# Kernel optimization log

Measured on AMD Instinct MI355X. Metric: run time of the kernel, lower is better.

## Reference

```python
import jax, jax.numpy as jnp
import numpy as np

FULL_SCALE = 32.0
TOPK = 5
R = 0.5


def _match(ca, cb, fa, fb):
    # ca: [Na,3] int coords, cb: [Nb,3] int coords, fa: [Na,C], fb: [Nb,C]
    xa = ca.astype(jnp.float32)
    xb = cb.astype(jnp.float32)
    # pairwise L2 distance via the expanded form, clamped at 0 before sqrt
    d2 = ((xa * xa).sum(-1)[:, None]
          + (xb * xb).sum(-1)[None, :]
          - 2.0 * (xa @ xb.T))                     # [Na, Nb]
    dist = jnp.sqrt(jnp.maximum(d2, 0.0)) / FULL_SCALE
    # smallest-k distances == top-k of negated distances
    neg_top, idx = jax.lax.top_k(-dist, TOPK)      # idx: [Na, TOPK]
    dist_w = R - jnp.clip(-neg_top, 0.0, R)        # [Na, TOPK]
    gathered = fb[idx]                             # [Na, TOPK, C]
    matched = jnp.sum(gathered * dist_w[..., None], axis=1)  # [Na, C]
    return jnp.concatenate([fa, matched], axis=-1)  # [Na, 2C]


def setup_inputs() -> dict:
    key = jax.random.key(0)
    k1, k2, k3, k4 = jax.random.split(key, 4)
    B, Na, Nb, C = 4, 8192, 8192, 64
    coords_a = jax.random.randint(k1, (B, Na, 3), 0, 32, dtype=jnp.int32)
    coords_b = jax.random.randint(k2, (B, Nb, 3), 0, 32, dtype=jnp.int32)
    feat_a = jax.random.normal(k3, (B, Na, C), dtype=jnp.float32)
    feat_b = jax.random.normal(k4, (B, Nb, C), dtype=jnp.float32)
    return {"coords_a": coords_a, "coords_b": coords_b,
            "feat_a": feat_a, "feat_b": feat_b}


def reference(coords_a, coords_b, feat_a, feat_b):
    # vmap over independent point groups (the original's python loop over batch idx)
    return jax.vmap(_match)(coords_a, coords_b, feat_a, feat_b)  # [B, Na, 2C]
```

## Files before the change

### kernel.cpp

```cpp
#include <hip/hip_runtime.h>
#include <stdint.h>


namespace {
constexpr int kB = 4;
constexpr int kNa = 8192;
constexpr int kNb = 8192;
constexpr int kC = 64;

constexpr int kRad = 8;
constexpr int kDMax = 64;
constexpr int kGrid = 48;
constexpr int kGrid2 = kGrid * kGrid;
constexpr int kGrid3 = kGrid2 * kGrid;
constexpr int kOff = kRad * kGrid2 + kRad * kGrid + kRad;

constexpr int kChunkSz = 32;
constexpr int kMaxChunks = 128;
constexpr int kTabCap = kMaxChunks * kChunkSz;

constexpr int kOvfCap = 256;

constexpr size_t kCntOff    = 0;
constexpr size_t kOvfCntOff = 442368;
constexpr size_t kOvfIdxOff = 442372;
constexpr size_t kSlotLoOff = 443396;
constexpr size_t kSlotHiOff = kSlotLoOff + (size_t)kB * kGrid3 * 4;
constexpr size_t kWsWords   = kSlotHiOff + (size_t)kB * kGrid3 * 4;
constexpr size_t kWsBytes   = kWsWords * 4ull;

constexpr int kZeroVecEnd = (int)((kOvfCntOff + 4) / 4);
constexpr int kFFVecBeg   = (int)(kSlotLoOff / 4);
constexpr int kFFVecEnd   = (int)(kSlotHiOff / 4);
constexpr int kClrBlocks  = (kFFVecEnd + 255) / 256;

struct Tab {
    uint32_t e[kTabCap];
    unsigned long long canStop[2];
    int nChunks;
};
constexpr Tab buildTab() {
    Tab t{};
    for (int i = 0; i < kTabCap; ++i) t.e[i] = 0x7FFFFFFFu;
    t.canStop[0] = 0; t.canStop[1] = 0;
    int cnt[kDMax + 1] = {};
    for (int dx = -kRad; dx <= kRad; ++dx)
        for (int dy = -kRad; dy <= kRad; ++dy)
            for (int dz = -kRad; dz <= kRad; ++dz) {
                const int d2 = dx * dx + dy * dy + dz * dz;
                if (d2 <= kDMax) cnt[d2]++;
            }
    int pos[kDMax + 1] = {};
    int fill = 0;
    for (int d = 0; d <= kDMax; ++d) {
        if (cnt[d] == 0) { pos[d] = -1; continue; }
        const int room = kChunkSz - (fill % kChunkSz);
        if (room < cnt[d] && room != kChunkSz) fill += room;
        pos[d] = fill;
        fill += cnt[d];
    }
    t.nChunks = (fill + kChunkSz - 1) / kChunkSz;
    for (int dx = -kRad; dx <= kRad; ++dx)
        for (int dy = -kRad; dy <= kRad; ++dy)
            for (int dz = -kRad; dz <= kRad; ++dz) {
                const int d2 = dx * dx + dy * dy + dz * dz;
                if (d2 <= kDMax) {
                    const int sd = dx * kGrid2 + dy * kGrid + dz + kOff;
                    t.e[pos[d2]++] = ((uint32_t)d2 << 18) | (uint32_t)sd;
                }
            }
    for (int c = 0; c < t.nChunks; ++c) {
        int lastReal = -1;
        for (int i = (c + 1) * kChunkSz - 1; i >= 0; --i) {
            const unsigned d = t.e[i] >> 18;
            if (d <= (unsigned)kDMax) { lastReal = (int)d; break; }
        }
        int nextReal = kDMax + 1;
        for (int i = (c + 1) * kChunkSz; i < kTabCap; ++i) {
            const unsigned d = t.e[i] >> 18;
            if (d <= (unsigned)kDMax) { nextReal = (int)d; break; }
        }
        if (nextReal > lastReal) t.canStop[c >> 6] |= (1ull << (c & 63));
    }
    return t;
}
__device__ constexpr Tab kTab = buildTab();
constexpr int kNChunks = buildTab().nChunks;
constexpr unsigned long long kCS0 = buildTab().canStop[0];
constexpr unsigned long long kCS1 = buildTab().canStop[1];
static_assert(buildTab().nChunks <= kMaxChunks, "table overflow");
}

__device__ __forceinline__ uint32_t umin_(uint32_t a, uint32_t b) { return a < b ? a : b; }
__device__ __forceinline__ uint32_t umax_(uint32_t a, uint32_t b) { return a > b ? a : b; }

#define INSERT5(T0, T1, T2, T3, T4, KEY) do {                 \
    const uint32_t m0_ = umax_(T0, KEY); T0 = umin_(T0, KEY); \
    const uint32_t m1_ = umax_(T1, m0_); T1 = umin_(T1, m0_); \
    const uint32_t m2_ = umax_(T2, m1_); T2 = umin_(T2, m1_); \
    const uint32_t m3_ = umax_(T3, m2_); T3 = umin_(T3, m2_); \
    T4 = umin_(T4, m3_); } while (0)

__device__ __forceinline__ void merge5_(uint32_t& t0, uint32_t& t1, uint32_t& t2,
                                        uint32_t& t3, uint32_t& t4,
                                        uint32_t b0, uint32_t b1, uint32_t b2,
                                        uint32_t b3, uint32_t b4) {
    const uint32_t c0 = umin_(t0, b0);
    const uint32_t c1 = umin_(umin_(umax_(t0, b0), t1), b1);
    const uint32_t c2 = umin_(umin_(umax_(t0, b1), umax_(t1, b0)), umin_(t2, b2));
    const uint32_t c3 = umin_(umin_(umax_(t0, b2), umax_(t1, b1)),
                              umin_(umax_(t2, b0), umin_(t3, b3)));
    const uint32_t c4 = umin_(umin_(umax_(t0, b3), umax_(t1, b2)),
                              umin_(umin_(umax_(t2, b1), umax_(t3, b0)),
                                    umin_(t4, b4)));
    t0 = c0; t1 = c1; t2 = c2; t3 = c3; t4 = c4;
}

__device__ __forceinline__ void groupMerge5_(uint32_t& t0, uint32_t& t1, uint32_t& t2,
                                             uint32_t& t3, uint32_t& t4) {
    #pragma unroll
    for (int s = 1; s < 16; s <<= 1) {
        const uint32_t b0 = (uint32_t)__shfl_xor((int)t0, s);
        const uint32_t b1 = (uint32_t)__shfl_xor((int)t1, s);
        const uint32_t b2 = (uint32_t)__shfl_xor((int)t2, s);
        const uint32_t b3 = (uint32_t)__shfl_xor((int)t3, s);
        const uint32_t b4 = (uint32_t)__shfl_xor((int)t4, s);
        merge5_(t0, t1, t2, t3, t4, b0, b1, b2, b3, b4);
    }
}

__device__ __forceinline__ void waveMerge5_(uint32_t& t0, uint32_t& t1, uint32_t& t2,
                                            uint32_t& t3, uint32_t& t4) {
    #pragma unroll
    for (int s = 1; s < 64; s <<= 1) {
        const uint32_t b0 = (uint32_t)__shfl_xor((int)t0, s);
        const uint32_t b1 = (uint32_t)__shfl_xor((int)t1, s);
        const uint32_t b2 = (uint32_t)__shfl_xor((int)t2, s);
        const uint32_t b3 = (uint32_t)__shfl_xor((int)t3, s);
        const uint32_t b4 = (uint32_t)__shfl_xor((int)t4, s);
        merge5_(t0, t1, t2, t3, t4, b0, b1, b2, b3, b4);
    }
}


__global__ __launch_bounds__(256)
void k_clear(uint4* __restrict__ ws) {
    const int i = blockIdx.x * 256 + threadIdx.x;
    if (i < kZeroVecEnd) ws[i] = uint4{0u, 0u, 0u, 0u};
    else if (i >= kFFVecBeg && i < kFFVecEnd) ws[i] = uint4{~0u, ~0u, ~0u, ~0u};
}

__global__ void k_scatter(const int* __restrict__ coords_b,
                          uint32_t* __restrict__ cnt,
                          uint32_t* __restrict__ slotLo,
                          uint32_t* __restrict__ slotHi,
                          uint32_t* __restrict__ ovfCnt,
                          uint32_t* __restrict__ ovfIdx) {
    const int i = blockIdx.x * blockDim.x + threadIdx.x;
    if (i >= kB * kNb) return;
    const int b = i >> 13;
    const int j = i & (kNb - 1);
    const int* p = coords_b + (size_t)i * 3;
    const int cell = b * kGrid3
                   + (p[0] + kRad) * kGrid2 + (p[1] + kRad) * kGrid + (p[2] + kRad);
    const uint32_t pos = atomicAdd(&cnt[cell], 1u);
    if (pos < 4u) {
        slotLo[(size_t)cell * 4 + pos] = (uint32_t)j;
    } else if (pos < 8u) {
        slotHi[(size_t)cell * 4 + (pos - 4u)] = (uint32_t)j;
    } else {
        const uint32_t op = atomicAdd(&ovfCnt[b], 1u);
        if (op < (uint32_t)kOvfCap) ovfIdx[b * kOvfCap + op] = (uint32_t)j;
    }
}


__global__ __launch_bounds__(512, 8)
void dist_match_bucket(const int* __restrict__ coords_a,
                       const int* __restrict__ coords_b,
                       const float* __restrict__ feat_a,
                       const float* __restrict__ feat_b,
                       const uint32_t* __restrict__ cnt,
                       const uint32_t* __restrict__ slotLo,
                       const uint32_t* __restrict__ slotHi,
                       const uint32_t* __restrict__ ovfCnt,
                       const uint32_t* __restrict__ ovfIdx,
                       float* __restrict__ out)
{
    const int b = blockIdx.x >> 8;
    const int rowBase = (blockIdx.x & 255) * 32;
    const int lane = threadIdx.x & 63;
    const int wave = threadIdx.x >> 6;
    const int sub = lane & 15;
    const int grp = lane >> 4;
    const int row = rowBase + wave * 4 + grp;

    const int* ca = coords_a + ((size_t)b * kNa + row) * 3;
    const int ax = ca[0], ay = ca[1], az = ca[2];
    const int aCell = (ax + kRad) * kGrid2 + (ay + kRad) * kGrid + (az + kRad);
    const int base = b * kGrid3 + aCell - kOff;

    uint32_t t0 = 0xFFFFFFFFu, t1 = t0, t2 = t0, t3 = t0, t4 = t0;
    int myCnt = 0;
    bool done = false;

    for (int c = 0; c < kNChunks; ++c) {
        if (__all(done)) break;
        if (!done) {
            const uint2 ee = *reinterpret_cast<const uint2*>(
                                 kTab.e + c * kChunkSz + sub * 2);
            const uint32_t d20 = ee.x >> 18, d21 = ee.y >> 18;
            const int cell0 = base + (int)(ee.x & 0x3FFFFu);
            const int cell1 = base + (int)(ee.y & 0x3FFFFu);
            uint4 s0 = uint4{~0u, ~0u, ~0u, ~0u};
            uint4 s1 = uint4{~0u, ~0u, ~0u, ~0u};
            if (d20 <= (uint32_t)kDMax)
                s0 = *reinterpret_cast<const uint4*>(slotLo + (size_t)cell0 * 4);
            if (d21 <= (uint32_t)kDMax)
                s1 = *reinterpret_cast<const uint4*>(slotLo + (size_t)cell1 * 4);

            const uint32_t kb0 = d20 << 13, kb1 = d21 << 13;
            INSERT5(t0, t1, t2, t3, t4, kb0 | s0.x);
            INSERT5(t0, t1, t2, t3, t4, kb0 | s0.y);
            INSERT5(t0, t1, t2, t3, t4, kb0 | s0.z);
            INSERT5(t0, t1, t2, t3, t4, kb0 | s0.w);
            INSERT5(t0, t1, t2, t3, t4, kb1 | s1.x);
            INSERT5(t0, t1, t2, t3, t4, kb1 | s1.y);
            INSERT5(t0, t1, t2, t3, t4, kb1 | s1.z);
            INSERT5(t0, t1, t2, t3, t4, kb1 | s1.w);

            myCnt += (s0.x != ~0u) + (s0.y != ~0u) + (s0.z != ~0u) + (s0.w != ~0u)
                   + (s1.x != ~0u) + (s1.y != ~0u) + (s1.z != ~0u) + (s1.w != ~0u);

            const uint32_t mx0 = umax_(umax_(s0.x, s0.y), umax_(s0.z, s0.w));
            const uint32_t mx1 = umax_(umax_(s1.x, s1.y), umax_(s1.z, s1.w));
            if (__any((mx0 != ~0u) | (mx1 != ~0u))) {
                if (mx0 != ~0u) {
                    const uint32_t n = umin_(cnt[cell0], 8u);
                    for (uint32_t m = 4; m < n; ++m)
                        INSERT5(t0, t1, t2, t3, t4,
                                kb0 | slotHi[(size_t)cell0 * 4 + (m - 4u)]);
                }
                if (mx1 != ~0u) {
                    const uint32_t n = umin_(cnt[cell1], 8u);
                    for (uint32_t m = 4; m < n; ++m)
                        INSERT5(t0, t1, t2, t3, t4,
                                kb1 | slotHi[(size_t)cell1 * 4 + (m - 4u)]);
                }
            }

            const bool canStop = (c < 64) ? (((kCS0 >> c) & 1ull) != 0)
                                          : (((kCS1 >> (c - 64)) & 1ull) != 0);
            if (canStop) {
                int gs = myCnt;
                gs += __shfl_xor(gs, 1);
                gs += __shfl_xor(gs, 2);
                gs += __shfl_xor(gs, 4);
                gs += __shfl_xor(gs, 8);
                if (gs >= 5) done = true;
            }
        }
    }

    groupMerge5_(t0, t1, t2, t3, t4);
    uint32_t g0 = t0, g1 = t1, g2 = t2, g3 = t3, g4 = t4;

    const uint32_t ovf = ovfCnt[b];
    bool needFull = (ovf > (uint32_t)kOvfCap);
    if (!needFull && ovf > 0) {
        const int* cb = coords_b + (size_t)b * kNb * 3;
        uint32_t l0 = 0xFFFFFFFFu, l1 = l0, l2 = l0, l3 = l0, l4 = l0;
        for (uint32_t i = (uint32_t)sub; i < ovf; i += 16) {
            const uint32_t j = ovfIdx[b * kOvfCap + i];
            const int dx = ax - cb[3 * j + 0];
            const int dy = ay - cb[3 * j + 1];
            const int dz = az - cb[3 * j + 2];
            const uint32_t d2 = (uint32_t)(dx * dx + dy * dy + dz * dz);
            INSERT5(l0, l1, l2, l3, l4, (d2 << 13) | j);
        }
        groupMerge5_(l0, l1, l2, l3, l4);
        merge5_(g0, g1, g2, g3, g4, l0, l1, l2, l3, l4);
    }
    if (!needFull && (g4 >> 13) > (uint32_t)kDMax) needFull = true;
    if (__any(needFull)) {
        if (needFull) {
            const int* cb = coords_b + (size_t)b * kNb * 3;
            uint32_t u0 = 0xFFFFFFFFu, u1 = u0, u2 = u0, u3 = u0, u4 = u0;
            for (int j = sub; j < kNb; j += 16) {
                const int dx = ax - cb[3 * j + 0];
                const int dy = ay - cb[3 * j + 1];
                const int dz = az - cb[3 * j + 2];
                const uint32_t d2 = (uint32_t)(dx * dx + dy * dy + dz * dz);
                INSERT5(u0, u1, u2, u3, u4, (d2 << 13) | (uint32_t)j);
            }
            groupMerge5_(u0, u1, u2, u3, u4);
            g0 = u0; g1 = u1; g2 = u2; g3 = u3; g4 = u4;
        }
    }

    const float* fb = feat_b + (size_t)b * kNb * kC;
    const uint32_t keys[5] = {g0, g1, g2, g3, g4};
    float4 acc = float4{0.f, 0.f, 0.f, 0.f};
    #pragma unroll
    for (int t = 0; t < 5; ++t) {
        const uint32_t key = keys[t];
        const int j = (int)(key & 8191u);
        const float dist = sqrtf((float)(key >> 13)) * (1.0f / 32.0f);
        const float w = 0.5f - fminf(dist, 0.5f);
        const float4 v = *reinterpret_cast<const float4*>(
                             fb + (size_t)j * kC + sub * 4);
        acc.x += w * v.x; acc.y += w * v.y; acc.z += w * v.z; acc.w += w * v.w;
    }

    const size_t arow = ((size_t)b * kNa + row) * kC;
    const float4 fa = *reinterpret_cast<const float4*>(feat_a + arow + sub * 4);
    const size_t orow = ((size_t)b * kNa + row) * (2 * kC);
    *reinterpret_cast<float4*>(out + orow + sub * 4) = fa;
    *reinterpret_cast<float4*>(out + orow + kC + sub * 4) = acc;
}


__global__ __launch_bounds__(512, 8)
void dist_match_brute(const int* __restrict__ coords_a,
                      const int* __restrict__ coords_b,
                      const float* __restrict__ feat_a,
                      const float* __restrict__ feat_b,
                      float* __restrict__ out)
{
    __shared__ int spack[kNb];
    const int b = blockIdx.x >> 10;
    const int rowBase = (blockIdx.x & 1023) * 8;
    const int tid = threadIdx.x;
    const int lane = tid & 63;
    const int wave = tid >> 6;

    const int* cb = coords_b + (size_t)b * kNb * 3;
    for (int j = tid; j < kNb; j += 512) {
        spack[j] = cb[3 * j + 0] | (cb[3 * j + 1] << 8) | (cb[3 * j + 2] << 16);
    }
    __syncthreads();

    const int row = rowBase + wave;
    const int* ca = coords_a + ((size_t)b * kNa + row) * 3;
    const int ax = ca[0], ay = ca[1], az = ca[2];
    const int a2 = ax * ax + ay * ay + az * az;
    const int paneg2 = ((-2 * ax) & 255) | (((-2 * ay) & 255) << 8)
                     | (((-2 * az) & 255) << 16);

    uint32_t t0 = 0xFFFFFFFFu, t1 = t0, t2 = t0, t3 = t0, t4 = t0;
    for (int k = 0; k < kNb / 256; ++k) {
        const int baseI = k * 256 + lane * 4;
        const int4 p4 = *reinterpret_cast<const int4*>(spack + baseI);
        const int ps[4] = {p4.x, p4.y, p4.z, p4.w};
        #pragma unroll
        for (int u = 0; u < 4; ++u) {
            const int p = ps[u];
            const int dot1 = __builtin_amdgcn_sdot4(paneg2, p, a2, false);
            const int d2 = __builtin_amdgcn_sdot4(p, p, dot1, false);
            const uint32_t key = ((uint32_t)d2 << 13) | (uint32_t)(baseI + u);
            INSERT5(t0, t1, t2, t3, t4, key);
        }
    }
    waveMerge5_(t0, t1, t2, t3, t4);
    const float* fb = feat_b + (size_t)b * kNb * kC;
    const uint32_t keys[5] = {t0, t1, t2, t3, t4};
    float acc = 0.0f;
    #pragma unroll
    for (int t = 0; t < 5; ++t) {
        const uint32_t key = keys[t];
        const int j = (int)(key & 8191u);
        const float dist = sqrtf((float)(key >> 13)) * (1.0f / 32.0f);
        const float w = 0.5f - fminf(dist, 0.5f);
        acc += w * fb[(size_t)j * kC + lane];
    }
    const size_t orow = ((size_t)b * kNa + row) * (2 * kC);
    out[orow + lane] = feat_a[((size_t)b * kNa + row) * kC + lane];
    out[orow + kC + lane] = acc;
}

extern "C" void kernel_launch(void* const* d_in, const int* in_sizes, int n_in,
                              void* d_out, int out_size, void* d_ws, size_t ws_size,
                              hipStream_t stream) {
    const int* coords_a = (const int*)d_in[0];
    const int* coords_b = (const int*)d_in[1];
    const float* feat_a = (const float*)d_in[2];
    const float* feat_b = (const float*)d_in[3];
    float* out = (float*)d_out;

    if (ws_size < kWsBytes) {
        dist_match_brute<<<kB * 1024, 512, 0, stream>>>(coords_a, coords_b,
                                                        feat_a, feat_b, out);
        return;
    }

    uint32_t* ws32 = (uint32_t*)d_ws;
    uint32_t* cnt    = ws32 + kCntOff;
    uint32_t* ovfCnt = ws32 + kOvfCntOff;
    uint32_t* ovfIdx = ws32 + kOvfIdxOff;
    uint32_t* slotLo = ws32 + kSlotLoOff;
    uint32_t* slotHi = ws32 + kSlotHiOff;

    k_clear<<<kClrBlocks, 256, 0, stream>>>((uint4*)d_ws);
    k_scatter<<<kB * kNb / 256, 256, 0, stream>>>(coords_b, cnt, slotLo, slotHi,
                                                  ovfCnt, ovfIdx);
    dist_match_bucket<<<kB * 256, 512, 0, stream>>>(coords_a, coords_b,
                                                    feat_a, feat_b,
                                                    cnt, slotLo, slotHi,
                                                    ovfCnt, ovfIdx, out);
}
```

Measured before the change: 30.88 us.

## Pack first four bucket slots as 16-bit indices and prefetch first two chunks

The first four slot indices per grid cell are now stored as 16-bit values instead of 32-bit, which halves the slot array and the bytes cleared and read per cell. The first two table chunks are loaded up front and processed without the generic loop, and the loop only runs if a group still has fewer than five candidates. The feat_a and overflow-count loads are hoisted to the kernel start so their latency overlaps the search. The sentinel 0xFFFF sign-extends to ~0, which preserves the empty-slot check but relies on indices staying below 65535.

```diff
diff --git a/kernel.cpp b/kernel.cpp
--- a/kernel.cpp
+++ b/kernel.cpp
@@ -24,13 +24,13 @@
 constexpr size_t kCntOff    = 0;
 constexpr size_t kOvfCntOff = 442368;
 constexpr size_t kOvfIdxOff = 442372;
-constexpr size_t kSlotLoOff = 443396;
-constexpr size_t kSlotHiOff = kSlotLoOff + (size_t)kB * kGrid3 * 4;
+constexpr size_t kSlot16Off = 443396;
+constexpr size_t kSlotHiOff = kSlot16Off + (size_t)kB * kGrid3 * 2;
 constexpr size_t kWsWords   = kSlotHiOff + (size_t)kB * kGrid3 * 4;
 constexpr size_t kWsBytes   = kWsWords * 4ull;
 
 constexpr int kZeroVecEnd = (int)((kOvfCntOff + 4) / 4);
-constexpr int kFFVecBeg   = (int)(kSlotLoOff / 4);
+constexpr int kFFVecBeg   = (int)(kSlot16Off / 4);
 constexpr int kFFVecEnd   = (int)(kSlotHiOff / 4);
 constexpr int kClrBlocks  = (kFFVecEnd + 255) / 256;
 
@@ -101,6 +101,13 @@
     const uint32_t m3_ = umax_(T3, m2_); T3 = umin_(T3, m2_); \
     T4 = umin_(T4, m3_); } while (0)
 
+#define UNPACK2_INS(W, KB, CNT) do {                                  \
+    const uint32_t v0_ = (uint32_t)(int32_t)(int16_t)((W) & 0xFFFFu); \
+    const uint32_t v1_ = (uint32_t)(int32_t)(int16_t)((W) >> 16);     \
+    INSERT5(t0, t1, t2, t3, t4, (KB) | v0_);                          \
+    INSERT5(t0, t1, t2, t3, t4, (KB) | v1_);                          \
+    CNT += (v0_ != ~0u) + (v1_ != ~0u); } while (0)
+
 __device__ __forceinline__ void merge5_(uint32_t& t0, uint32_t& t1, uint32_t& t2,
                                         uint32_t& t3, uint32_t& t4,
                                         uint32_t b0, uint32_t b1, uint32_t b2,
@@ -142,6 +149,14 @@
     }
 }
 
+__device__ __forceinline__ int groupSum16_(int v) {
+    v += __shfl_xor(v, 1);
+    v += __shfl_xor(v, 2);
+    v += __shfl_xor(v, 4);
+    v += __shfl_xor(v, 8);
+    return v;
+}
+
 
 __global__ __launch_bounds__(256)
 void k_clear(uint4* __restrict__ ws) {
@@ -152,7 +167,7 @@
 
 __global__ void k_scatter(const int* __restrict__ coords_b,
                           uint32_t* __restrict__ cnt,
-                          uint32_t* __restrict__ slotLo,
+                          uint16_t* __restrict__ slot16,
                           uint32_t* __restrict__ slotHi,
                           uint32_t* __restrict__ ovfCnt,
                           uint32_t* __restrict__ ovfIdx) {
@@ -165,7 +180,7 @@
                    + (p[0] + kRad) * kGrid2 + (p[1] + kRad) * kGrid + (p[2] + kRad);
     const uint32_t pos = atomicAdd(&cnt[cell], 1u);
     if (pos < 4u) {
-        slotLo[(size_t)cell * 4 + pos] = (uint32_t)j;
+        slot16[(size_t)cell * 4 + pos] = (uint16_t)j;
     } else if (pos < 8u) {
         slotHi[(size_t)cell * 4 + (pos - 4u)] = (uint32_t)j;
     } else {
@@ -181,7 +196,7 @@
                        const float* __restrict__ feat_a,
                        const float* __restrict__ feat_b,
                        const uint32_t* __restrict__ cnt,
-                       const uint32_t* __restrict__ slotLo,
+                       const uint16_t* __restrict__ slot16,
                        const uint32_t* __restrict__ slotHi,
                        const uint32_t* __restrict__ ovfCnt,
                        const uint32_t* __restrict__ ovfIdx,
@@ -195,6 +210,10 @@
     const int grp = lane >> 4;
     const int row = rowBase + wave * 4 + grp;
 
+    const uint32_t ovf = ovfCnt[b];
+    const size_t arow = ((size_t)b * kNa + row) * kC;
+    const float4 fa = *reinterpret_cast<const float4*>(feat_a + arow + sub * 4);
+
     const int* ca = coords_a + ((size_t)b * kNa + row) * 3;
     const int ax = ca[0], ay = ca[1], az = ca[2];
     const int aCell = (ax + kRad) * kGrid2 + (ay + kRad) * kGrid + (az + kRad);
@@ -202,62 +221,112 @@
 
     uint32_t t0 = 0xFFFFFFFFu, t1 = t0, t2 = t0, t3 = t0, t4 = t0;
     int myCnt = 0;
-    bool done = false;
-
-    for (int c = 0; c < kNChunks; ++c) {
-        if (__all(done)) break;
-        if (!done) {
-            const uint2 ee = *reinterpret_cast<const uint2*>(
-                                 kTab.e + c * kChunkSz + sub * 2);
-            const uint32_t d20 = ee.x >> 18, d21 = ee.y >> 18;
-            const int cell0 = base + (int)(ee.x & 0x3FFFFu);
-            const int cell1 = base + (int)(ee.y & 0x3FFFFu);
-            uint4 s0 = uint4{~0u, ~0u, ~0u, ~0u};
-            uint4 s1 = uint4{~0u, ~0u, ~0u, ~0u};
-            if (d20 <= (uint32_t)kDMax)
-                s0 = *reinterpret_cast<const uint4*>(slotLo + (size_t)cell0 * 4);
-            if (d21 <= (uint32_t)kDMax)
-                s1 = *reinterpret_cast<const uint4*>(slotLo + (size_t)cell1 * 4);
-
-            const uint32_t kb0 = d20 << 13, kb1 = d21 << 13;
-            INSERT5(t0, t1, t2, t3, t4, kb0 | s0.x);
-            INSERT5(t0, t1, t2, t3, t4, kb0 | s0.y);
-            INSERT5(t0, t1, t2, t3, t4, kb0 | s0.z);
-            INSERT5(t0, t1, t2, t3, t4, kb0 | s0.w);
-            INSERT5(t0, t1, t2, t3, t4, kb1 | s1.x);
-            INSERT5(t0, t1, t2, t3, t4, kb1 | s1.y);
-            INSERT5(t0, t1, t2, t3, t4, kb1 | s1.z);
-            INSERT5(t0, t1, t2, t3, t4, kb1 | s1.w);
-
-            myCnt += (s0.x != ~0u) + (s0.y != ~0u) + (s0.z != ~0u) + (s0.w != ~0u)
-                   + (s1.x != ~0u) + (s1.y != ~0u) + (s1.z != ~0u) + (s1.w != ~0u);
-
-            const uint32_t mx0 = umax_(umax_(s0.x, s0.y), umax_(s0.z, s0.w));
-            const uint32_t mx1 = umax_(umax_(s1.x, s1.y), umax_(s1.z, s1.w));
-            if (__any((mx0 != ~0u) | (mx1 != ~0u))) {
-                if (mx0 != ~0u) {
-                    const uint32_t n = umin_(cnt[cell0], 8u);
+
+    const uint2 eA = *reinterpret_cast<const uint2*>(kTab.e + sub * 2);
+    const uint2 eB = *reinterpret_cast<const uint2*>(kTab.e + kChunkSz + sub * 2);
+    const uint32_t dA0 = eA.x >> 18, dA1 = eA.y >> 18;
+    const uint32_t dB0 = eB.x >> 18, dB1 = eB.y >> 18;
+    const int cA0 = base + (int)(eA.x & 0x3FFFFu);
+    const int cA1 = base + (int)(eA.y & 0x3FFFFu);
+    const int cB0 = base + (int)(eB.x & 0x3FFFFu);
+    const int cB1 = base + (int)(eB.y & 0x3FFFFu);
+    uint2 sA0 = uint2{~0u, ~0u}, sA1 = sA0, sB0 = sA0, sB1 = sA0;
+    if (dA0 <= (uint32_t)kDMax)
+        sA0 = *reinterpret_cast<const uint2*>(slot16 + (size_t)cA0 * 4);
+    if (dA1 <= (uint32_t)kDMax)
+        sA1 = *reinterpret_cast<const uint2*>(slot16 + (size_t)cA1 * 4);
+    if (dB0 <= (uint32_t)kDMax)
+        sB0 = *reinterpret_cast<const uint2*>(slot16 + (size_t)cB0 * 4);
+    if (dB1 <= (uint32_t)kDMax)
+        sB1 = *reinterpret_cast<const uint2*>(slot16 + (size_t)cB1 * 4);
+
+    const uint32_t kbA0 = dA0 << 13, kbA1 = dA1 << 13;
+    const uint32_t kbB0 = dB0 << 13, kbB1 = dB1 << 13;
+
+    UNPACK2_INS(sA0.x, kbA0, myCnt); UNPACK2_INS(sA0.y, kbA0, myCnt);
+    UNPACK2_INS(sA1.x, kbA1, myCnt); UNPACK2_INS(sA1.y, kbA1, myCnt);
+    const bool fullA0 = (sA0.y >> 16) != 0xFFFFu;
+    const bool fullA1 = (sA1.y >> 16) != 0xFFFFu;
+    if (__any(fullA0 | fullA1)) {
+        if (fullA0) {
+            const uint32_t n = umin_(cnt[cA0], 8u);
+            for (uint32_t m = 4; m < n; ++m)
+                INSERT5(t0, t1, t2, t3, t4, kbA0 | slotHi[(size_t)cA0 * 4 + (m - 4u)]);
+        }
+        if (fullA1) {
+            const uint32_t n = umin_(cnt[cA1], 8u);
+            for (uint32_t m = 4; m < n; ++m)
+                INSERT5(t0, t1, t2, t3, t4, kbA1 | slotHi[(size_t)cA1 * 4 + (m - 4u)]);
+        }
+    }
+
+    int gs = groupSum16_(myCnt);
+    bool doneG = (gs >= 5);
+
+    if (__any(!doneG)) {
+        if (!doneG) {
+            UNPACK2_INS(sB0.x, kbB0, myCnt); UNPACK2_INS(sB0.y, kbB0, myCnt);
+            UNPACK2_INS(sB1.x, kbB1, myCnt); UNPACK2_INS(sB1.y, kbB1, myCnt);
+            const bool fullB0 = (sB0.y >> 16) != 0xFFFFu;
+            const bool fullB1 = (sB1.y >> 16) != 0xFFFFu;
+            if (__any(fullB0 | fullB1)) {
+                if (fullB0) {
+                    const uint32_t n = umin_(cnt[cB0], 8u);
                     for (uint32_t m = 4; m < n; ++m)
-                        INSERT5(t0, t1, t2, t3, t4,
-                                kb0 | slotHi[(size_t)cell0 * 4 + (m - 4u)]);
+                        INSERT5(t0, t1, t2, t3, t4, kbB0 | slotHi[(size_t)cB0 * 4 + (m - 4u)]);
                 }
-                if (mx1 != ~0u) {
-                    const uint32_t n = umin_(cnt[cell1], 8u);
+                if (fullB1) {
+                    const uint32_t n = umin_(cnt[cB1], 8u);
                     for (uint32_t m = 4; m < n; ++m)
-                        INSERT5(t0, t1, t2, t3, t4,
-                                kb1 | slotHi[(size_t)cell1 * 4 + (m - 4u)]);
+                        INSERT5(t0, t1, t2, t3, t4, kbB1 | slotHi[(size_t)cB1 * 4 + (m - 4u)]);
                 }
             }
-
-            const bool canStop = (c < 64) ? (((kCS0 >> c) & 1ull) != 0)
-                                          : (((kCS1 >> (c - 64)) & 1ull) != 0);
-            if (canStop) {
-                int gs = myCnt;
-                gs += __shfl_xor(gs, 1);
-                gs += __shfl_xor(gs, 2);
-                gs += __shfl_xor(gs, 4);
-                gs += __shfl_xor(gs, 8);
-                if (gs >= 5) done = true;
+            gs = groupSum16_(myCnt);
+            doneG = (gs >= 5);
+        } else {
+            doneG = true;
+        }
+    }
+
+    if (__any(!doneG)) {
+        bool done = doneG;
+        for (int c = 2; c < kNChunks; ++c) {
+            if (__all(done)) break;
+            if (!done) {
+                const uint2 ee = *reinterpret_cast<const uint2*>(
+                                     kTab.e + c * kChunkSz + sub * 2);
+                const uint32_t d20 = ee.x >> 18, d21 = ee.y >> 18;
+                const int cell0 = base + (int)(ee.x & 0x3FFFFu);
+                const int cell1 = base + (int)(ee.y & 0x3FFFFu);
+                uint2 s0 = uint2{~0u, ~0u}, s1 = s0;
+                if (d20 <= (uint32_t)kDMax)
+                    s0 = *reinterpret_cast<const uint2*>(slot16 + (size_t)cell0 * 4);
+                if (d21 <= (uint32_t)kDMax)
+                    s1 = *reinterpret_cast<const uint2*>(slot16 + (size_t)cell1 * 4);
+                const uint32_t kb0 = d20 << 13, kb1 = d21 << 13;
+                UNPACK2_INS(s0.x, kb0, myCnt); UNPACK2_INS(s0.y, kb0, myCnt);
+                UNPACK2_INS(s1.x, kb1, myCnt); UNPACK2_INS(s1.y, kb1, myCnt);
+                const bool full0 = (s0.y >> 16) != 0xFFFFu;
+                const bool full1 = (s1.y >> 16) != 0xFFFFu;
+                if (__any(full0 | full1)) {
+                    if (full0) {
+                        const uint32_t n = umin_(cnt[cell0], 8u);
+                        for (uint32_t m = 4; m < n; ++m)
+                            INSERT5(t0, t1, t2, t3, t4,
+                                    kb0 | slotHi[(size_t)cell0 * 4 + (m - 4u)]);
+                    }
+                    if (full1) {
+                        const uint32_t n = umin_(cnt[cell1], 8u);
+                        for (uint32_t m = 4; m < n; ++m)
+                            INSERT5(t0, t1, t2, t3, t4,
+                                    kb1 | slotHi[(size_t)cell1 * 4 + (m - 4u)]);
+                    }
+                }
+                const bool canStop = (c < 64) ? (((kCS0 >> c) & 1ull) != 0)
+                                              : (((kCS1 >> (c - 64)) & 1ull) != 0);
+                if (canStop) {
+                    if (groupSum16_(myCnt) >= 5) done = true;
+                }
             }
         }
     }
@@ -265,7 +334,6 @@
     groupMerge5_(t0, t1, t2, t3, t4);
     uint32_t g0 = t0, g1 = t1, g2 = t2, g3 = t3, g4 = t4;
 
-    const uint32_t ovf = ovfCnt[b];
     bool needFull = (ovf > (uint32_t)kOvfCap);
     if (!needFull && ovf > 0) {
         const int* cb = coords_b + (size_t)b * kNb * 3;
@@ -312,8 +380,6 @@
         acc.x += w * v.x; acc.y += w * v.y; acc.z += w * v.z; acc.w += w * v.w;
     }
 
-    const size_t arow = ((size_t)b * kNa + row) * kC;
-    const float4 fa = *reinterpret_cast<const float4*>(feat_a + arow + sub * 4);
     const size_t orow = ((size_t)b * kNa + row) * (2 * kC);
     *reinterpret_cast<float4*>(out + orow + sub * 4) = fa;
     *reinterpret_cast<float4*>(out + orow + kC + sub * 4) = acc;
@@ -397,14 +463,14 @@
     uint32_t* cnt    = ws32 + kCntOff;
     uint32_t* ovfCnt = ws32 + kOvfCntOff;
     uint32_t* ovfIdx = ws32 + kOvfIdxOff;
-    uint32_t* slotLo = ws32 + kSlotLoOff;
+    uint16_t* slot16 = (uint16_t*)(ws32 + kSlot16Off);
     uint32_t* slotHi = ws32 + kSlotHiOff;
 
     k_clear<<<kClrBlocks, 256, 0, stream>>>((uint4*)d_ws);
-    k_scatter<<<kB * kNb / 256, 256, 0, stream>>>(coords_b, cnt, slotLo, slotHi,
+    k_scatter<<<kB * kNb / 256, 256, 0, stream>>>(coords_b, cnt, slot16, slotHi,
                                                   ovfCnt, ovfIdx);
     dist_match_bucket<<<kB * 256, 512, 0, stream>>>(coords_a, coords_b,
                                                     feat_a, feat_b,
-                                                    cnt, slotLo, slotHi,
+                                                    cnt, slot16, slotHi,
                                                     ovfCnt, ovfIdx, out);
 }
```

Result: no change. 30.52 us (-1.1%).
